# Performance work log

Measured on AMD Instinct MI355X. Metric: run time of the kernel, lower is better.

The kernel has to match this reference:

```python
import jax, jax.numpy as jnp
import numpy as np

EMB = 1024
HEADS = 16
HEAD_DIM = EMB // HEADS
B, S = 4, 2048


def setup_inputs() -> dict:
    key = jax.random.key(0)
    ks = jax.random.split(key, 7)
    sc = 1.0 / np.sqrt(EMB)
    return {
        "query": jax.random.normal(ks[0], (B, S, EMB), jnp.float32),
        "key": jax.random.normal(ks[1], (B, S, EMB), jnp.float32),
        "value": jax.random.normal(ks[2], (B, S, EMB), jnp.float32),
        "Wq": jax.random.normal(ks[3], (EMB, EMB), jnp.float32) * sc,
        "Wk": jax.random.normal(ks[4], (EMB, EMB), jnp.float32) * sc,
        "Wv": jax.random.normal(ks[5], (EMB, EMB), jnp.float32) * sc,
        "Wo": jax.random.normal(ks[6], (EMB, EMB), jnp.float32) * sc,
    }


def reference(query, key, value, Wq, Wk, Wv, Wo):
    # nn.Linear applies x @ W^T; W stored as [out, in]
    def split_heads(x):  # [B,S,E] -> [B,H,S,D]
        return x.reshape(B, -1, HEADS, HEAD_DIM).transpose(0, 2, 1, 3)

    q = split_heads(query @ Wq.T)
    k = split_heads(key @ Wk.T)
    v = split_heads(value @ Wv.T)
    scores = jnp.einsum('bhse,bhte->bhst', q, k) / np.sqrt(HEAD_DIM).astype(np.float32)
    attn = jax.nn.softmax(scores, axis=-1)
    ctx = jnp.einsum('bhst,bhtd->bshd', attn, v)  # [B,S,H,D]
    out = ctx.reshape(B, -1, EMB) @ Wo.T
    return out
```

## Files before the change

### kernel.cpp

```cpp
#include <hip/hip_runtime.h>
#include <hip/hip_bf16.h>

#define EMB   1024
#define HEADS 16
#define HDIM  64
#define BB    4
#define SS    2048
#define MROWS (BB*SS)

typedef __bf16 bf16_t;
typedef __bf16 bf16x4_t __attribute__((ext_vector_type(4)));
typedef __bf16 bf16x8   __attribute__((ext_vector_type(8)));
typedef float  f32x4    __attribute__((ext_vector_type(4)));

__device__ __forceinline__ void glds16(const void* g, void* l) {
  __builtin_amdgcn_global_load_lds(
      (const __attribute__((address_space(1))) void*)g,
      (__attribute__((address_space(3))) void*)l, 16, 0, 0);
}

__launch_bounds__(256)
__global__ void cast_multi(const float* s0, const float* s1, const float* s2,
                           const float* s3, const float* s4, const float* s5,
                           const float* s6,
                           bf16_t* d0, bf16_t* d1, bf16_t* d2, bf16_t* d3,
                           bf16_t* d4, bf16_t* d5, bf16_t* d6, int nact) {
  const int z = blockIdx.z;
  if (z >= nact && blockIdx.x >= 512) return;
  const float* ss[7] = {s0, s1, s2, s3, s4, s5, s6};
  bf16_t*      dd[7] = {d0, d1, d2, d3, d4, d5, d6};
  const float* s = ss[z];
  bf16_t*      d = dd[z];
  const int i = (blockIdx.x*256 + threadIdx.x) * 8;
  const f32x4 a = *(const f32x4*)&s[i];
  const f32x4 b = *(const f32x4*)&s[i+4];
  bf16x8 r;
  r[0]=(bf16_t)a[0]; r[1]=(bf16_t)a[1]; r[2]=(bf16_t)a[2]; r[3]=(bf16_t)a[3];
  r[4]=(bf16_t)b[0]; r[5]=(bf16_t)b[1]; r[6]=(bf16_t)b[2]; r[7]=(bf16_t)b[3];
  *(bf16x8*)&d[i] = r;
}

__launch_bounds__(256)
__global__ void cast_f32_bf16(const float* __restrict__ src, bf16_t* __restrict__ dst) {
  const int i = (blockIdx.x*256 + threadIdx.x) * 8;
  const f32x4 a = *(const f32x4*)&src[i];
  const f32x4 b = *(const f32x4*)&src[i+4];
  bf16x8 r;
  r[0]=(bf16_t)a[0]; r[1]=(bf16_t)a[1]; r[2]=(bf16_t)a[2]; r[3]=(bf16_t)a[3];
  r[4]=(bf16_t)b[0]; r[5]=(bf16_t)b[1]; r[6]=(bf16_t)b[2]; r[7]=(bf16_t)b[3];
  *(bf16x8*)&dst[i] = r;
}

__device__ __forceinline__ void gemm_core(const bf16_t* __restrict__ A,
                                          const bf16_t* __restrict__ W,
                                          bf16_t* As, bf16_t* Bs,
                                          f32x4 acc[4][4],
                                          int bm0, int bn0,
                                          int wave, int lane) {
  const int quad = lane >> 4, l16 = lane & 15;
  const int wm = wave >> 1, wn = wave & 1;
  for (int k0 = 0; k0 < EMB; k0 += 32) {
#pragma unroll
    for (int j = 0; j < 2; ++j) {
      const int i   = wave*2 + j;
      const int row = i*16 + (lane >> 2);
      const int col = (lane & 3) * 8;
      glds16(A + (size_t)(bm0 + row)*EMB + k0 + col, &As[i*512]);
      glds16(W + (size_t)(bn0 + row)*EMB + k0 + col, &Bs[i*512]);
    }
    __syncthreads();

    bf16x8 a[4], b[4];
#pragma unroll
    for (int t = 0; t < 4; ++t) {
      a[t] = *(const bf16x8*)&As[(wm*64 + t*16 + l16)*32 + quad*8];
      b[t] = *(const bf16x8*)&Bs[(wn*64 + t*16 + l16)*32 + quad*8];
    }
#pragma unroll
    for (int mt = 0; mt < 4; ++mt)
#pragma unroll
      for (int nt = 0; nt < 4; ++nt)
        acc[mt][nt] = __builtin_amdgcn_mfma_f32_16x16x32_bf16(a[mt], b[nt], acc[mt][nt], 0, 0, 0);
    __syncthreads();
  }
}

__launch_bounds__(256)
__global__ void gemm_qkv(const bf16_t* A0, const bf16_t* A1, const bf16_t* A2,
                         const bf16_t* W0, const bf16_t* W1, const bf16_t* W2,
                         bf16_t* C0, bf16_t* C1, bf16_t* C2,
                         float sscale, int zbase) {
  __shared__ __align__(16) bf16_t As[128*32];
  __shared__ __align__(16) bf16_t Bs[128*32];
  const int tid  = threadIdx.x;
  const int wave = tid >> 6, lane = tid & 63;
  const int quad = lane >> 4, l16 = lane & 15;
  const int wm = wave >> 1, wn = wave & 1;

  const int fid = blockIdx.x + 8*(blockIdx.y + 64*blockIdx.z);
  const int xcd = fid & 7, s = fid >> 3;
  const int bn0 = (s & 7) * 128;
  const int p   = xcd + 8*(s >> 3);
  const int z   = (p >> 6) + zbase;
  const int bm0 = (p & 63) * 128;

  const bf16_t* A = (z == 0) ? A0 : (z == 1) ? A1 : A2;
  const bf16_t* W = (z == 0) ? W0 : (z == 1) ? W1 : W2;
  bf16_t*       C = (z == 0) ? C0 : (z == 1) ? C1 : C2;
  const float oscale = (z == 0) ? sscale : 1.0f;

  f32x4 acc[4][4] = {};
  gemm_core(A, W, As, Bs, acc, bm0, bn0, wave, lane);

  if (z == 2) {
    const int bb = bm0 >> 11;
    const int T  = ((bm0 & 2047) >> 6) + wm;
    const int h  = (bn0 >> 6) + wn;
    bf16_t* base = C + ((size_t)(bb*HEADS + h)*32 + T)*4096;
#pragma unroll
    for (int ks = 0; ks < 2; ++ks)
#pragma unroll
      for (int nt = 0; nt < 4; ++nt) {
        bf16x8 v;
#pragma unroll
        for (int r = 0; r < 4; ++r) {
          v[r]     = (bf16_t)acc[2*ks][nt][r];
          v[4 + r] = (bf16_t)acc[2*ks + 1][nt][r];
        }
        *(bf16x8*)&base[((nt*2 + ks)*64 + quad*16 + l16)*8] = v;
      }
  } else {
#pragma unroll
    for (int mt = 0; mt < 4; ++mt) {
      const int row = bm0 + wm*64 + mt*16 + quad*4;
#pragma unroll
      for (int nt = 0; nt < 4; ++nt) {
        const int col = bn0 + wn*64 + nt*16 + l16;
#pragma unroll
        for (int r = 0; r < 4; ++r)
          C[(size_t)(row + r)*EMB + col] = (bf16_t)(acc[mt][nt][r] * oscale);
      }
    }
  }
}

__launch_bounds__(256)
__global__ void gemm_out(const bf16_t* __restrict__ A, const bf16_t* __restrict__ W,
                         float* __restrict__ C) {
  __shared__ __align__(16) bf16_t As[128*32];
  __shared__ __align__(16) bf16_t Bs[128*32];
  const int tid  = threadIdx.x;
  const int wave = tid >> 6, lane = tid & 63;
  const int quad = lane >> 4, l16 = lane & 15;
  const int wm = wave >> 1, wn = wave & 1;

  const int fid = blockIdx.x + 8*blockIdx.y;
  const int xcd = fid & 7, s = fid >> 3;
  const int bn0 = (s & 7) * 128;
  const int bm0 = (xcd*8 + (s >> 3)) * 128;

  f32x4 acc[4][4] = {};
  gemm_core(A, W, As, Bs, acc, bm0, bn0, wave, lane);

#pragma unroll
  for (int mt = 0; mt < 4; ++mt) {
    const int row = bm0 + wm*64 + mt*16 + quad*4;
#pragma unroll
    for (int nt = 0; nt < 4; ++nt) {
      const int col = bn0 + wn*64 + nt*16 + l16;
#pragma unroll
      for (int r = 0; r < 4; ++r)
        C[(size_t)(row + r)*EMB + col] = acc[mt][nt][r];
    }
  }
}

__launch_bounds__(256)
__global__ void attn(const bf16_t* Qp, const bf16_t* __restrict__ Kp,
                     const bf16_t* __restrict__ Vt, bf16_t* Cx) {
  __shared__ __align__(16) bf16_t Ks[2][4096];
  __shared__ __align__(16) bf16_t Vs[2][4096];

  const int tid  = threadIdx.x;
  const int wave = tid >> 6, lane = tid & 63;
  const int quad = lane >> 4, l16 = lane & 15;

  const int fid  = blockIdx.x + 16*(blockIdx.y + 16*blockIdx.z);
  const int xcd  = fid & 7, s = fid >> 3;
  const int q0   = (s & 15) * 128;
  const int pair = xcd*8 + (s >> 4);
  const int h    = pair & 15;
  const int b    = pair >> 4;

  bf16x8 qf[2][2];
#pragma unroll
  for (int mb = 0; mb < 2; ++mb) {
    const size_t qr = (size_t)(b*SS + q0 + wave*32 + mb*16 + l16)*EMB + h*HDIM;
#pragma unroll
    for (int ks = 0; ks < 2; ++ks)
      qf[mb][ks] = *(const bf16x8*)&Qp[qr + ks*32 + quad*8];
  }

  const bf16_t* Kb = Kp + (size_t)b*SS*EMB + h*HDIM;
  const bf16_t* Vb = Vt + ((size_t)(b*HEADS + h)*32)*4096;

  f32x4 o[2][4] = {};
  f32x4 lsv[2] = {};

  auto stage = [&](int t0, int bf) {
#pragma unroll
    for (int c = 0; c < 2; ++c) {
      const int i = wave + c*4;
      glds16(Kb + (size_t)(t0 + (i&3)*16 + l16)*EMB + (i>>2)*32 + quad*8,
             &Ks[bf][i*512]);
      glds16(Vb + (size_t)(t0 >> 6)*4096 + i*512 + lane*8, &Vs[bf][i*512]);
    }
  };

  stage(0, 0);

  for (int t0 = 0, buf = 0; t0 < SS; t0 += 64, buf ^= 1) {
    __syncthreads();
    if (t0 + 64 < SS) stage(t0 + 64, buf ^ 1);

    f32x4 st[2][4] = {};
#pragma unroll
    for (int cb = 0; cb < 4; ++cb) {
      const bf16x8 kf0 = *(const bf16x8*)&Ks[buf][cb*512 + lane*8];
      const bf16x8 kf1 = *(const bf16x8*)&Ks[buf][2048 + cb*512 + lane*8];
#pragma unroll
      for (int mb = 0; mb < 2; ++mb) {
        st[mb][cb] = __builtin_amdgcn_mfma_f32_16x16x32_bf16(kf0, qf[mb][0], st[mb][cb], 0, 0, 0);
        st[mb][cb] = __builtin_amdgcn_mfma_f32_16x16x32_bf16(kf1, qf[mb][1], st[mb][cb], 0, 0, 0);
      }
    }

    bf16x8 pb[2][2];
#pragma unroll
    for (int mb = 0; mb < 2; ++mb) {
#pragma unroll
      for (int kb = 0; kb < 4; ++kb) {
#pragma unroll
        for (int r = 0; r < 4; ++r)
          st[mb][kb][r] = __builtin_amdgcn_exp2f(st[mb][kb][r]);
        lsv[mb] += st[mb][kb];
      }
#pragma unroll
      for (int ks = 0; ks < 2; ++ks)
#pragma unroll
        for (int r = 0; r < 4; ++r) {
          pb[mb][ks][r]     = (bf16_t)st[mb][2*ks][r];
          pb[mb][ks][4 + r] = (bf16_t)st[mb][2*ks + 1][r];
        }
    }

#pragma unroll
    for (int ks = 0; ks < 2; ++ks)
#pragma unroll
      for (int dt = 0; dt < 4; ++dt) {
        const bf16x8 vf = *(const bf16x8*)&Vs[buf][((dt*2 + ks)*64 + lane)*8];
#pragma unroll
        for (int mb = 0; mb < 2; ++mb)
          o[mb][dt] = __builtin_amdgcn_mfma_f32_16x16x32_bf16(vf, pb[mb][ks], o[mb][dt], 0, 0, 0);
      }
  }

#pragma unroll
  for (int mb = 0; mb < 2; ++mb) {
    float l = lsv[mb][0] + lsv[mb][1] + lsv[mb][2] + lsv[mb][3];
    l += __shfl_xor(l, 16, 64);
    l += __shfl_xor(l, 32, 64);
    const float inv = 1.0f / l;
    const size_t row = (size_t)(b*SS + q0 + wave*32 + mb*16 + l16)*EMB + h*HDIM;
#pragma unroll
    for (int dt = 0; dt < 4; ++dt) {
      bf16x4_t v;
#pragma unroll
      for (int r = 0; r < 4; ++r) v[r] = (bf16_t)(o[mb][dt][r] * inv);
      *(bf16x4_t*)&Cx[row + dt*16 + quad*4] = v;
    }
  }
}

extern "C" void kernel_launch(void* const* d_in, const int* in_sizes, int n_in,
                              void* d_out, int out_size, void* d_ws, size_t ws_size,
                              hipStream_t stream) {
  (void)in_sizes; (void)n_in; (void)out_size;
  const float* query = (const float*)d_in[0];
  const float* key   = (const float*)d_in[1];
  const float* value = (const float*)d_in[2];
  const float* WqF   = (const float*)d_in[3];
  const float* WkF   = (const float*)d_in[4];
  const float* WvF   = (const float*)d_in[5];
  const float* WoF   = (const float*)d_in[6];

  const size_t AN = (size_t)MROWS*EMB;
  const size_t WN = (size_t)EMB*EMB;
  float* out = (float*)d_out;
  bf16_t* S5 = (bf16_t*)d_out;
  bf16_t* S6 = S5 + AN;

  const float sscale = 0.125f * 1.44269504f;

  const dim3 gqkv(EMB/128, MROWS/128, 3);
  const dim3 gqk (EMB/128, MROWS/128, 2);
  const dim3 gv  (EMB/128, MROWS/128, 1);
  const dim3 gg  (EMB/128, MROWS/128);
  const dim3 gattn(SS/128, HEADS, BB);

  if (ws_size >= (size_t)(4*AN + 4*WN) * sizeof(bf16_t)) {
    bf16_t* qb  = (bf16_t*)d_ws;
    bf16_t* kb  = qb + AN;
    bf16_t* vb  = kb + AN;
    bf16_t* S2  = vb + AN;
    bf16_t* Wqb = S2 + AN;
    bf16_t* Wkb = Wqb + WN;
    bf16_t* Wvb = Wkb + WN;
    bf16_t* Wob = Wvb + WN;

    cast_multi<<<dim3(AN/2048, 1, 7), 256, 0, stream>>>(
        query, key, value, WqF, WkF, WvF, WoF,
        qb, kb, vb, Wqb, Wkb, Wvb, Wob, 3);
    gemm_qkv<<<gqkv, 256, 0, stream>>>(qb, kb, vb, Wqb, Wkb, Wvb,
                                       S2, S6, S5, sscale, 0);
    attn<<<gattn, 256, 0, stream>>>(S2, S6, S5, S2);
    gemm_out<<<gg, 256, 0, stream>>>(S2, Wob, out);
  } else {
    bf16_t* S1  = (bf16_t*)d_ws;
    bf16_t* S2  = S1 + AN;
    bf16_t* Wqb = S2 + AN;
    bf16_t* Wkb = Wqb + WN;
    bf16_t* Wvb = Wkb + WN;
    bf16_t* Wob = Wvb + WN;

    cast_multi<<<dim3(AN/2048, 1, 6), 256, 0, stream>>>(
        query, key, WqF, WkF, WvF, WoF, WoF,
        S1, S5, Wqb, Wkb, Wvb, Wob, Wob, 2);
    gemm_qkv<<<gqk, 256, 0, stream>>>(S1, S5, S1, Wqb, Wkb, Wvb,
                                      S2, S6, S5, sscale, 0);
    cast_f32_bf16<<<dim3(AN/2048), 256, 0, stream>>>(value, S1);
    gemm_qkv<<<gv, 256, 0, stream>>>(S1, S1, S1, Wvb, Wvb, Wvb,
                                     S5, S5, S5, 1.0f, 2);
    attn<<<gattn, 256, 0, stream>>>(S2, S6, S5, S2);
    gemm_out<<<gg, 256, 0, stream>>>(S2, Wob, out);
  }
}
```

Measured before the change: 321.6 us.

## Software-pipeline attention loop: overlap next QK and softmax with current PV

Restructures the flash-attention inner loop so the QK^T MFMAs for the next tile are issued together with the PV MFMAs of the current tile, and the exp/softmax of the next tile runs after the next tile's loads are issued. s_setprio is raised around the MFMA block to favour the matrix work. The aim is to hide exp (transcendental) latency and LDS loads behind MFMA work. In exchange it adds a second barrier per iteration and more live registers.

```diff
diff --git a/kernel.cpp b/kernel.cpp
--- a/kernel.cpp
+++ b/kernel.cpp
@@ -206,36 +206,33 @@
 
   f32x4 o[2][4] = {};
   f32x4 lsv[2] = {};
-
-  auto stage = [&](int t0, int bf) {
+  bf16x8 pb[2][2];
+
+  auto stage = [&](int ti, int bf) {
+    const int t0 = ti * 64;
 #pragma unroll
     for (int c = 0; c < 2; ++c) {
       const int i = wave + c*4;
       glds16(Kb + (size_t)(t0 + (i&3)*16 + l16)*EMB + (i>>2)*32 + quad*8,
              &Ks[bf][i*512]);
-      glds16(Vb + (size_t)(t0 >> 6)*4096 + i*512 + lane*8, &Vs[bf][i*512]);
+      glds16(Vb + (size_t)ti*4096 + i*512 + lane*8, &Vs[bf][i*512]);
     }
   };
 
-  stage(0, 0);
-
-  for (int t0 = 0, buf = 0; t0 < SS; t0 += 64, buf ^= 1) {
-    __syncthreads();
-    if (t0 + 64 < SS) stage(t0 + 64, buf ^ 1);
-
-    f32x4 st[2][4] = {};
+  auto QK = [&](int bf, f32x4 (&st)[2][4]) {
 #pragma unroll
     for (int cb = 0; cb < 4; ++cb) {
-      const bf16x8 kf0 = *(const bf16x8*)&Ks[buf][cb*512 + lane*8];
-      const bf16x8 kf1 = *(const bf16x8*)&Ks[buf][2048 + cb*512 + lane*8];
+      const bf16x8 kf0 = *(const bf16x8*)&Ks[bf][cb*512 + lane*8];
+      const bf16x8 kf1 = *(const bf16x8*)&Ks[bf][2048 + cb*512 + lane*8];
 #pragma unroll
       for (int mb = 0; mb < 2; ++mb) {
         st[mb][cb] = __builtin_amdgcn_mfma_f32_16x16x32_bf16(kf0, qf[mb][0], st[mb][cb], 0, 0, 0);
         st[mb][cb] = __builtin_amdgcn_mfma_f32_16x16x32_bf16(kf1, qf[mb][1], st[mb][cb], 0, 0, 0);
       }
     }
-
-    bf16x8 pb[2][2];
+  };
+
+  auto SM = [&](f32x4 (&st)[2][4]) {
 #pragma unroll
     for (int mb = 0; mb < 2; ++mb) {
 #pragma unroll
@@ -253,17 +250,44 @@
           pb[mb][ks][4 + r] = (bf16_t)st[mb][2*ks + 1][r];
         }
     }
-
+  };
+
+  auto PV = [&](int bf) {
 #pragma unroll
     for (int ks = 0; ks < 2; ++ks)
 #pragma unroll
       for (int dt = 0; dt < 4; ++dt) {
-        const bf16x8 vf = *(const bf16x8*)&Vs[buf][((dt*2 + ks)*64 + lane)*8];
+        const bf16x8 vf = *(const bf16x8*)&Vs[bf][((dt*2 + ks)*64 + lane)*8];
 #pragma unroll
         for (int mb = 0; mb < 2; ++mb)
           o[mb][dt] = __builtin_amdgcn_mfma_f32_16x16x32_bf16(vf, pb[mb][ks], o[mb][dt], 0, 0, 0);
       }
-  }
+  };
+
+  stage(0, 0);
+  __syncthreads();
+  stage(1, 1);
+  {
+    f32x4 st[2][4] = {};
+    QK(0, st);
+    SM(st);
+  }
+
+  const int NT = SS / 64;
+  for (int t = 0; t < NT - 1; ++t) {
+    const int buf = t & 1;
+    __syncthreads();
+    __builtin_amdgcn_s_setprio(1);
+    f32x4 stn[2][4] = {};
+    QK(buf ^ 1, stn);
+    PV(buf);
+    __builtin_amdgcn_s_setprio(0);
+    __syncthreads();
+    if (t + 2 < NT) stage(t + 2, buf);
+    SM(stn);
+  }
+
+  PV((NT - 1) & 1);
 
 #pragma unroll
   for (int mb = 0; mb < 2; ++mb) {
```

Result: slower. 332.6 us (+3.4%).

## Use 8 waves per attention block, each owning 16 query rows

Applied to the files above, without the earlier changes.

The attention kernel moves from 4 waves handling 32 query rows each to 8 waves handling 16 rows each. Each wave now stages one K and one V chunk per tile instead of two, and register use for the score and output accumulators is halved. The goal is higher occupancy and more latency hiding. In exchange, the MFMA work per LDS read of K and V drops, so each K/V fragment feeds one MFMA instead of two, and more waves contend at each barrier.

```diff
diff --git a/kernel.cpp b/kernel.cpp
--- a/kernel.cpp
+++ b/kernel.cpp
@@ -175,7 +175,7 @@
   }
 }
 
-__launch_bounds__(256)
+__launch_bounds__(512, 8)
 __global__ void attn(const bf16_t* Qp, const bf16_t* __restrict__ Kp,
                      const bf16_t* __restrict__ Vt, bf16_t* Cx) {
   __shared__ __align__(16) bf16_t Ks[2][4096];
@@ -192,93 +192,79 @@
   const int h    = pair & 15;
   const int b    = pair >> 4;
 
-  bf16x8 qf[2][2];
-#pragma unroll
-  for (int mb = 0; mb < 2; ++mb) {
-    const size_t qr = (size_t)(b*SS + q0 + wave*32 + mb*16 + l16)*EMB + h*HDIM;
-#pragma unroll
-    for (int ks = 0; ks < 2; ++ks)
-      qf[mb][ks] = *(const bf16x8*)&Qp[qr + ks*32 + quad*8];
+  bf16x8 qf[2];
+  {
+    const size_t qr = (size_t)(b*SS + q0 + wave*16 + l16)*EMB + h*HDIM;
+    qf[0] = *(const bf16x8*)&Qp[qr + quad*8];
+    qf[1] = *(const bf16x8*)&Qp[qr + 32 + quad*8];
   }
 
   const bf16_t* Kb = Kp + (size_t)b*SS*EMB + h*HDIM;
   const bf16_t* Vb = Vt + ((size_t)(b*HEADS + h)*32)*4096;
 
-  f32x4 o[2][4] = {};
-  f32x4 lsv[2] = {};
-
-  auto stage = [&](int t0, int bf) {
-#pragma unroll
-    for (int c = 0; c < 2; ++c) {
-      const int i = wave + c*4;
-      glds16(Kb + (size_t)(t0 + (i&3)*16 + l16)*EMB + (i>>2)*32 + quad*8,
-             &Ks[bf][i*512]);
-      glds16(Vb + (size_t)(t0 >> 6)*4096 + i*512 + lane*8, &Vs[bf][i*512]);
-    }
+  f32x4 o[4] = {};
+  f32x4 lsv = {};
+
+  auto stage = [&](int ti, int bf) {
+    const int t0 = ti * 64;
+    const int i  = wave;
+    glds16(Kb + (size_t)(t0 + (i&3)*16 + l16)*EMB + (i>>2)*32 + quad*8,
+           &Ks[bf][i*512]);
+    glds16(Vb + (size_t)ti*4096 + i*512 + lane*8, &Vs[bf][i*512]);
   };
 
   stage(0, 0);
 
-  for (int t0 = 0, buf = 0; t0 < SS; t0 += 64, buf ^= 1) {
+  const int NT = SS / 64;
+  for (int t = 0, buf = 0; t < NT; ++t, buf ^= 1) {
     __syncthreads();
-    if (t0 + 64 < SS) stage(t0 + 64, buf ^ 1);
-
-    f32x4 st[2][4] = {};
+    if (t + 1 < NT) stage(t + 1, buf ^ 1);
+
+    f32x4 st[4] = {};
 #pragma unroll
     for (int cb = 0; cb < 4; ++cb) {
       const bf16x8 kf0 = *(const bf16x8*)&Ks[buf][cb*512 + lane*8];
       const bf16x8 kf1 = *(const bf16x8*)&Ks[buf][2048 + cb*512 + lane*8];
-#pragma unroll
-      for (int mb = 0; mb < 2; ++mb) {
-        st[mb][cb] = __builtin_amdgcn_mfma_f32_16x16x32_bf16(kf0, qf[mb][0], st[mb][cb], 0, 0, 0);
-        st[mb][cb] = __builtin_amdgcn_mfma_f32_16x16x32_bf16(kf1, qf[mb][1], st[mb][cb], 0, 0, 0);
+      st[cb] = __builtin_amdgcn_mfma_f32_16x16x32_bf16(kf0, qf[0], st[cb], 0, 0, 0);
+      st[cb] = __builtin_amdgcn_mfma_f32_16x16x32_bf16(kf1, qf[1], st[cb], 0, 0, 0);
+    }
+
+#pragma unroll
+    for (int kb = 0; kb < 4; ++kb) {
+#pragma unroll
+      for (int r = 0; r < 4; ++r)
+        st[kb][r] = __builtin_amdgcn_exp2f(st[kb][r]);
+      lsv += st[kb];
+    }
+    bf16x8 pb[2];
+#pragma unroll
+    for (int ks = 0; ks < 2; ++ks)
+#pragma unroll
+      for (int r = 0; r < 4; ++r) {
+        pb[ks][r]     = (bf16_t)st[2*ks][r];
+        pb[ks][4 + r] = (bf16_t)st[2*ks + 1][r];
       }
-    }
-
-    bf16x8 pb[2][2];
-#pragma unroll
-    for (int mb = 0; mb < 2; ++mb) {
-#pragma unroll
-      for (int kb = 0; kb < 4; ++kb) {
-#pragma unroll
-        for (int r = 0; r < 4; ++r)
-          st[mb][kb][r] = __builtin_amdgcn_exp2f(st[mb][kb][r]);
-        lsv[mb] += st[mb][kb];
-      }
-#pragma unroll
-      for (int ks = 0; ks < 2; ++ks)
-#pragma unroll
-        for (int r = 0; r < 4; ++r) {
-          pb[mb][ks][r]     = (bf16_t)st[mb][2*ks][r];
-          pb[mb][ks][4 + r] = (bf16_t)st[mb][2*ks + 1][r];
-        }
-    }
 
 #pragma unroll
     for (int ks = 0; ks < 2; ++ks)
 #pragma unroll
       for (int dt = 0; dt < 4; ++dt) {
         const bf16x8 vf = *(const bf16x8*)&Vs[buf][((dt*2 + ks)*64 + lane)*8];
-#pragma unroll
-        for (int mb = 0; mb < 2; ++mb)
-          o[mb][dt] = __builtin_amdgcn_mfma_f32_16x16x32_bf16(vf, pb[mb][ks], o[mb][dt], 0, 0, 0);
+        o[dt] = __builtin_amdgcn_mfma_f32_16x16x32_bf16(vf, pb[ks], o[dt], 0, 0, 0);
       }
   }
 
-#pragma unroll
-  for (int mb = 0; mb < 2; ++mb) {
-    float l = lsv[mb][0] + lsv[mb][1] + lsv[mb][2] + lsv[mb][3];
-    l += __shfl_xor(l, 16, 64);
-    l += __shfl_xor(l, 32, 64);
-    const float inv = 1.0f / l;
-    const size_t row = (size_t)(b*SS + q0 + wave*32 + mb*16 + l16)*EMB + h*HDIM;
-#pragma unroll
-    for (int dt = 0; dt < 4; ++dt) {
-      bf16x4_t v;
-#pragma unroll
-      for (int r = 0; r < 4; ++r) v[r] = (bf16_t)(o[mb][dt][r] * inv);
-      *(bf16x4_t*)&Cx[row + dt*16 + quad*4] = v;
-    }
+  float l = lsv[0] + lsv[1] + lsv[2] + lsv[3];
+  l += __shfl_xor(l, 16, 64);
+  l += __shfl_xor(l, 32, 64);
+  const float inv = 1.0f / l;
+  const size_t row = (size_t)(b*SS + q0 + wave*16 + l16)*EMB + h*HDIM;
+#pragma unroll
+  for (int dt = 0; dt < 4; ++dt) {
+    bf16x4_t v;
+#pragma unroll
+    for (int r = 0; r < 4; ++r) v[r] = (bf16_t)(o[dt][r] * inv);
+    *(bf16x4_t*)&Cx[row + dt*16 + quad*4] = v;
   }
 }
 
@@ -323,7 +309,7 @@
         qb, kb, vb, Wqb, Wkb, Wvb, Wob, 3);
     gemm_qkv<<<gqkv, 256, 0, stream>>>(qb, kb, vb, Wqb, Wkb, Wvb,
                                        S2, S6, S5, sscale, 0);
-    attn<<<gattn, 256, 0, stream>>>(S2, S6, S5, S2);
+    attn<<<gattn, 512, 0, stream>>>(S2, S6, S5, S2);
     gemm_out<<<gg, 256, 0, stream>>>(S2, Wob, out);
   } else {
     bf16_t* S1  = (bf16_t*)d_ws;
@@ -341,7 +327,7 @@
     cast_f32_bf16<<<dim3(AN/2048), 256, 0, stream>>>(value, S1);
     gemm_qkv<<<gv, 256, 0, stream>>>(S1, S1, S1, Wvb, Wvb, Wvb,
                                      S5, S5, S5, 1.0f, 2);
-    attn<<<gattn, 256, 0, stream>>>(S2, S6, S5, S2);
+    attn<<<gattn, 512, 0, stream>>>(S2, S6, S5, S2);
     gemm_out<<<gg, 256, 0, stream>>>(S2, Wob, out);
   }
 }
```

Result: no change. 325.3 us (+1.1%).
